# Optimization experiments

Hardware: AMD Instinct MI355X
Metric: run time of the kernel (lower is better)

## Reference

```python
import jax, jax.numpy as jnp
import numpy as np

E = 800_000    # num elements
N = 400_000    # num nodes
NEN = 3        # nodes per element (linear triangle)
NQP = 1        # quadrature points per element
NST = 1        # state variables per quad point
DT = 0.0
MATS = ((1.0, 0.5), (2.0, 1.0))  # (lam, mu) for block0, block1


def _element_energy(elDisp, elCoords, elState, elShapes, elShapeGrads, elVols, lam, mu):
    # FunctionSpace.integrate_element_from_local_field with a Neo-Hookean
    # Lagrangian L(U, gradU, Q, X, dt) = W(gradU, Q); modify_element_gradient = identity.
    def qp(shape, grad, vol, Q):
        gradU = jnp.einsum('nc,nd->cd', elDisp, grad)            # [2,2] displacement gradient
        F = jnp.eye(2, dtype=elDisp.dtype) + gradU
        J = F[0, 0] * F[1, 1] - F[0, 1] * F[1, 0]
        logJ = jnp.log(J)
        I1 = jnp.sum(F * F)
        mu_eff = mu * (1.0 + 0.01 * Q[0])                        # internal variable modulates stiffness
        W = 0.5 * mu_eff * (I1 - 2.0 - 2.0 * logJ) + 0.5 * lam * logJ * logJ
        return W * vol
    return jnp.sum(jax.vmap(qp)(elShapes, elShapeGrads, elVols, elState))


def _block_hessians(U, coords, state, conns, shapes, shapeGrads, vols, elemIds, lam, mu):
    # gather per-block element fields, hessian-of-energy per element, vmapped
    def elem(elConn, elState, elShapes, elShapeGrads, elVols):
        elCoords = coords[elConn]                                # [NEN,2]
        f = lambda d: _element_energy(d, elCoords, elState, elShapes, elShapeGrads, elVols, lam, mu)
        return jax.hessian(f)(U[elConn])                         # [NEN,2,NEN,2]
    return jax.vmap(elem)(conns[elemIds], state[elemIds], shapes[elemIds],
                          shapeGrads[elemIds], vols[elemIds])


def setup_inputs() -> dict:
    key = jax.random.key(0)
    ks = jax.random.split(key, 8)
    U = 0.01 * jax.random.normal(ks[0], (N, 2), jnp.float32)     # small disp -> det(F) > 0
    coords = jax.random.uniform(ks[1], (N, 2), dtype=jnp.float32)
    state = jax.random.uniform(ks[2], (E, NQP, NST), dtype=jnp.float32)
    conns = jax.random.randint(ks[3], (E, NEN), 0, N, dtype=jnp.int32)
    shapes = jax.random.uniform(ks[4], (E, NQP, NEN), dtype=jnp.float32)
    shapeGrads = jax.random.normal(ks[5], (E, NQP, NEN, 2), jnp.float32)
    vols = jax.random.uniform(ks[6], (E, NQP), dtype=jnp.float32)
    perm = jax.random.permutation(ks[7], E)                      # disjoint material blocks
    blocks0 = perm[: E // 2].astype(jnp.int32)
    blocks1 = perm[E // 2:].astype(jnp.int32)
    return dict(U=U, coords=coords, state=state, conns=conns, shapes=shapes,
                shapeGrads=shapeGrads, vols=vols, blocks0=blocks0, blocks1=blocks1)


def reference(U, coords, state, conns, shapes, shapeGrads, vols, blocks0, blocks1):
    # compute_element_stiffnesses: gather -> per-element hessian -> scatter per block
    hess = jnp.zeros((E, NEN, 2, NEN, 2), dtype=U.dtype)
    for blk, (lam, mu) in zip((blocks0, blocks1), MATS):
        bh = _block_hessians(U, coords, state, conns, shapes, shapeGrads, vols, blk, lam, mu)
        hess = hess.at[blk].set(bh)
    return hess
```

## Files before the change

kernel.cpp:

```cpp
#include <hip/hip_runtime.h>


constexpr int E_CNT  = 800000;
constexpr int HALF_E = 400000;

__global__ __launch_bounds__(256) void mark_blocks_kernel(
    const int* __restrict__ b0, const int* __restrict__ b1,
    unsigned char* __restrict__ flag) {
  int i = blockIdx.x * blockDim.x + threadIdx.x;
  if (i < HALF_E) {
    flag[b0[i]] = 0;
    flag[b1[i]] = 1;
  }
}

__global__ __launch_bounds__(256) void hess_kernel(
    const float* __restrict__ U, const float* __restrict__ state,
    const int* __restrict__ conns, const float* __restrict__ grads,
    const float* __restrict__ vols, const unsigned char* __restrict__ flag,
    float* __restrict__ out) {
  int e = blockIdx.x * blockDim.x + threadIdx.x;
  if (e >= E_CNT) return;

  const bool b  = flag[e] != 0;
  const float lam = b ? 2.0f : 1.0f;
  const float mu  = b ? 1.0f : 0.5f;

  const int n0 = conns[3 * e + 0];
  const int n1 = conns[3 * e + 1];
  const int n2 = conns[3 * e + 2];
  const float2 d0 = *(const float2*)(U + 2 * n0);
  const float2 d1 = *(const float2*)(U + 2 * n1);
  const float2 d2 = *(const float2*)(U + 2 * n2);
  const float2* gp = (const float2*)(grads + 6 * e);
  const float2 g0 = gp[0], g1 = gp[1], g2 = gp[2];

  const float gu00 = d0.x * g0.x + d1.x * g1.x + d2.x * g2.x;
  const float gu01 = d0.x * g0.y + d1.x * g1.y + d2.x * g2.y;
  const float gu10 = d0.y * g0.x + d1.y * g1.x + d2.y * g2.x;
  const float gu11 = d0.y * g0.y + d1.y * g1.y + d2.y * g2.y;

  const float F00 = 1.0f + gu00, F01 = gu01, F10 = gu10, F11 = 1.0f + gu11;
  const float J    = F00 * F11 - F01 * F10;
  const float logJ = logf(J);
  const float rJ   = 1.0f / J;
  const float Fi00 =  F11 * rJ, Fi01 = -F01 * rJ;
  const float Fi10 = -F10 * rJ, Fi11 =  F00 * rJ;

  float P[3][2];
  P[0][0] = g0.x * Fi00 + g0.y * Fi10;  P[0][1] = g0.x * Fi01 + g0.y * Fi11;
  P[1][0] = g1.x * Fi00 + g1.y * Fi10;  P[1][1] = g1.x * Fi01 + g1.y * Fi11;
  P[2][0] = g2.x * Fi00 + g2.y * Fi10;  P[2][1] = g2.x * Fi01 + g2.y * Fi11;

  const float gx[3] = {g0.x, g1.x, g2.x};
  const float gy[3] = {g0.y, g1.y, g2.y};

  const float mu_eff = mu * (1.0f + 0.01f * state[e]);
  const float c2     = mu_eff - lam * logJ;
  const float vol    = vols[e];

  float h[36];
#pragma unroll
  for (int n = 0; n < 3; ++n) {
#pragma unroll
    for (int m = 0; m < 3; ++m) {
      const float dg = gx[n] * gx[m] + gy[n] * gy[m];
#pragma unroll
      for (int c = 0; c < 2; ++c) {
#pragma unroll
        for (int d = 0; d < 2; ++d) {
          float v = c2 * P[n][d] * P[m][c] + lam * P[n][c] * P[m][d];
          if (c == d) v += mu_eff * dg;
          h[n * 12 + c * 6 + m * 2 + d] = vol * v;
        }
      }
    }
  }

  float4* op = (float4*)(out + 36 * e);
#pragma unroll
  for (int i = 0; i < 9; ++i)
    op[i] = make_float4(h[4 * i + 0], h[4 * i + 1], h[4 * i + 2], h[4 * i + 3]);
}

extern "C" void kernel_launch(void* const* d_in, const int* in_sizes, int n_in,
                              void* d_out, int out_size, void* d_ws, size_t ws_size,
                              hipStream_t stream) {
  const float* U     = (const float*)d_in[0];
  const float* state = (const float*)d_in[2];
  const int*   conns = (const int*)d_in[3];
  const float* grads = (const float*)d_in[5];
  const float* vols  = (const float*)d_in[6];
  const int*   b0    = (const int*)d_in[7];
  const int*   b1    = (const int*)d_in[8];
  float* out = (float*)d_out;
  unsigned char* flag = (unsigned char*)d_ws;

  mark_blocks_kernel<<<(HALF_E + 255) / 256, 256, 0, stream>>>(b0, b1, flag);
  hess_kernel<<<(E_CNT + 255) / 256, 256, 0, stream>>>(U, state, conns, grads,
                                                       vols, flag, out);
}
```

Baseline: 217.9 us.

## Stage hessian output through LDS for coalesced stores; replace block marking with zero-fill

Each thread now writes its 36 hessian entries into shared memory, padded to a 37-float stride to avoid bank conflicts. After a barrier, the block writes its whole output tile with consecutive float4 stores, replacing per-thread strided 144-byte writes. The flag setup becomes a vectorized zero-fill plus one scatter over block1 indices, dropping the scatter over block0. The cost is about 37 KB of LDS per block, which may limit occupancy, plus an extra barrier and index divisions. The bounds check is removed, relying on E being a multiple of 256.

```diff
diff --git a/kernel.cpp b/kernel.cpp
--- a/kernel.cpp
+++ b/kernel.cpp
@@ -4,14 +4,15 @@
 constexpr int E_CNT  = 800000;
 constexpr int HALF_E = 400000;
 
-__global__ __launch_bounds__(256) void mark_blocks_kernel(
-    const int* __restrict__ b0, const int* __restrict__ b1,
-    unsigned char* __restrict__ flag) {
+__global__ __launch_bounds__(256) void zero_flags_kernel(uint4* __restrict__ flag4) {
   int i = blockIdx.x * blockDim.x + threadIdx.x;
-  if (i < HALF_E) {
-    flag[b0[i]] = 0;
-    flag[b1[i]] = 1;
-  }
+  if (i < E_CNT / 16) flag4[i] = make_uint4(0, 0, 0, 0);
+}
+
+__global__ __launch_bounds__(256) void mark_b1_kernel(
+    const int* __restrict__ b1, unsigned char* __restrict__ flag) {
+  int i = blockIdx.x * blockDim.x + threadIdx.x;
+  if (i < HALF_E) flag[b1[i]] = 1;
 }
 
 __global__ __launch_bounds__(256) void hess_kernel(
@@ -19,8 +20,9 @@
     const int* __restrict__ conns, const float* __restrict__ grads,
     const float* __restrict__ vols, const unsigned char* __restrict__ flag,
     float* __restrict__ out) {
-  int e = blockIdx.x * blockDim.x + threadIdx.x;
-  if (e >= E_CNT) return;
+  __shared__ float lds[256 * 37];
+  const int tid = threadIdx.x;
+  const int e = blockIdx.x * 256 + tid;
 
   const bool b  = flag[e] != 0;
   const float lam = b ? 2.0f : 1.0f;
@@ -59,7 +61,7 @@
   const float c2     = mu_eff - lam * logJ;
   const float vol    = vols[e];
 
-  float h[36];
+  float* hl = lds + tid * 37;
 #pragma unroll
   for (int n = 0; n < 3; ++n) {
 #pragma unroll
@@ -71,16 +73,25 @@
         for (int d = 0; d < 2; ++d) {
           float v = c2 * P[n][d] * P[m][c] + lam * P[n][c] * P[m][d];
           if (c == d) v += mu_eff * dg;
-          h[n * 12 + c * 6 + m * 2 + d] = vol * v;
+          hl[n * 12 + c * 6 + m * 2 + d] = vol * v;
         }
       }
     }
   }
 
-  float4* op = (float4*)(out + 36 * e);
+  __syncthreads();
+
+  float4* ob = (float4*)(out + 36 * (size_t)(blockIdx.x * 256));
 #pragma unroll
-  for (int i = 0; i < 9; ++i)
-    op[i] = make_float4(h[4 * i + 0], h[4 * i + 1], h[4 * i + 2], h[4 * i + 3]);
+  for (int i = 0; i < 9; ++i) {
+    const int f = 4 * (tid + i * 256);
+    float4 v;
+    v.x = lds[(f + 0) + (f + 0) / 36];
+    v.y = lds[(f + 1) + (f + 1) / 36];
+    v.z = lds[(f + 2) + (f + 2) / 36];
+    v.w = lds[(f + 3) + (f + 3) / 36];
+    ob[tid + i * 256] = v;
+  }
 }
 
 extern "C" void kernel_launch(void* const* d_in, const int* in_sizes, int n_in,
@@ -91,12 +102,12 @@
   const int*   conns = (const int*)d_in[3];
   const float* grads = (const float*)d_in[5];
   const float* vols  = (const float*)d_in[6];
-  const int*   b0    = (const int*)d_in[7];
   const int*   b1    = (const int*)d_in[8];
   float* out = (float*)d_out;
   unsigned char* flag = (unsigned char*)d_ws;
 
-  mark_blocks_kernel<<<(HALF_E + 255) / 256, 256, 0, stream>>>(b0, b1, flag);
-  hess_kernel<<<(E_CNT + 255) / 256, 256, 0, stream>>>(U, state, conns, grads,
-                                                       vols, flag, out);
+  zero_flags_kernel<<<(E_CNT / 16 + 255) / 256, 256, 0, stream>>>((uint4*)flag);
+  mark_b1_kernel<<<(HALF_E + 255) / 256, 256, 0, stream>>>(b1, flag);
+  hess_kernel<<<E_CNT / 256, 256, 0, stream>>>(U, state, conns, grads,
+                                               vols, flag, out);
 }
```

Measured after the change: 190.5 us. -12.5%, faster.
